# Performance work log

Measured on AMD Instinct MI355X. Metric: run time of the kernel, lower is better.

Reference implementation:

```python
import jax, jax.numpy as jnp
import numpy as np

IMAGE_SIZE = 128
FACES_PER_PIXEL = 4
BLUR_RADIUS = 0.01
EPS = 1e-8


def setup_inputs() -> dict:
    key = jax.random.key(0)
    k1, k2, k3 = jax.random.split(key, 3)
    B, V, F = 2, 2000, 800
    # verts are already projected to screen/NDC space: x,y in [-1,1], z > 0 (depth)
    xy = jax.random.uniform(k1, (B, V, 2), minval=-1.0, maxval=1.0)
    z = jax.random.uniform(k2, (B, V, 1), minval=0.5, maxval=2.5)
    verts = jnp.concatenate([xy, z], axis=-1).astype(jnp.float32)
    faces = jax.random.randint(k3, (F, 3), 0, V)
    return {"verts": verts, "faces": faces}


def _edge(a, b, p):
    # signed parallelogram area of (a -> b -> p), using xy components only
    return (p[..., 0] - a[..., 0]) * (b[..., 1] - a[..., 1]) - (
        p[..., 1] - a[..., 1]) * (b[..., 0] - a[..., 0])


def _seg_dist2(p, a, b):
    # squared distance from point p to segment [a, b] in 2D
    ab = b - a
    pa = p - a
    t = jnp.clip(jnp.sum(pa * ab, -1) / (jnp.sum(ab * ab, -1) + EPS), 0.0, 1.0)
    d = pa - t[..., None] * ab
    return jnp.sum(d * d, -1)


def _rasterize(verts, faces):
    H = W = IMAGE_SIZE
    K = FACES_PER_PIXEL
    B = verts.shape[0]
    fv = verts[:, faces]                      # [B,F,3,3] gather face vertices
    v0, v1, v2 = fv[:, :, 0], fv[:, :, 1], fv[:, :, 2]
    a0 = v0[:, None, :, :2]                   # [B,1,F,2]
    a1 = v1[:, None, :, :2]
    a2 = v2[:, None, :, :2]
    z0 = v0[:, None, :, 2]                    # [B,1,F]
    z1 = v1[:, None, :, 2]
    z2 = v2[:, None, :, 2]
    # pixel centers in NDC, pytorch3d convention: index 0 -> +1, last -> -1
    xs = 1.0 - 2.0 * (jnp.arange(W, dtype=verts.dtype) + 0.5) / W
    ys = 1.0 - 2.0 * (jnp.arange(H, dtype=verts.dtype) + 0.5) / H
    yy, xx = jnp.meshgrid(ys, xs, indexing="ij")
    p = jnp.stack([xx, yy], -1).reshape(1, -1, 1, 2)   # [1,P,1,2], P=H*W

    area = _edge(a0, a1, a2)                  # [B,1,F] signed face area*2
    w0 = _edge(a1, a2, p)                     # [B,P,F]
    w1 = _edge(a2, a0, p)
    w2 = _edge(a0, a1, p)
    denom = jnp.where(jnp.abs(area) > EPS, area,
                      jnp.where(area >= 0, EPS, -EPS))
    b0, b1, b2 = w0 / denom, w1 / denom, w2 / denom
    zpix = b0 * z0 + b1 * z1 + b2 * z2        # [B,P,F] interpolated depth

    inside = (b0 >= 0) & (b1 >= 0) & (b2 >= 0)
    dmin = jnp.minimum(_seg_dist2(p, a0, a1),
                       jnp.minimum(_seg_dist2(p, a1, a2),
                                   _seg_dist2(p, a2, a0)))
    dsign = jnp.where(inside, -dmin, dmin)    # signed squared edge distance

    valid = (inside | (dmin < BLUR_RADIUS)) & (zpix > EPS) & (
        jnp.abs(area) > EPS)
    zcand = jnp.where(valid, zpix, jnp.inf)
    _, idx = jax.lax.top_k(-zcand, K)         # K nearest faces per pixel

    take = lambda x: jnp.take_along_axis(x, idx, axis=-1)
    sel_valid = take(valid)
    pix_to_face = jnp.where(sel_valid, idx, -1)
    zbuf = jnp.where(sel_valid, take(zpix), -1.0)
    bary = jnp.stack([b0, b1, b2], -1)        # [B,P,F,3]
    bsel = jnp.take_along_axis(bary, idx[..., None], axis=2)  # [B,P,K,3]
    bsel = jnp.where(sel_valid[..., None], bsel, -1.0)
    dsel = jnp.where(sel_valid, take(dsign), -1.0)

    return (pix_to_face.reshape(B, H, W, K),
            zbuf.reshape(B, H, W, K),
            bsel.reshape(B, H, W, K, 3),
            dsel.reshape(B, H, W, K))


def reference(verts, faces):
    # Fragments: (pix_to_face, zbuf, bary_coords, dists)
    return _rasterize(verts, faces)
```

## Files before the change

kernel.cpp:

```cpp
#include <hip/hip_runtime.h>

#define IMG   128
#define KF    4
#define NF    800
#define NV    2000
#define NB    2
#define EPSF  1e-8f
#define BLURF 0.01f
#define CULL_D2 0.0103f
#define HEXT    0.0547f

typedef unsigned long long u64;
#define INVK ((((u64)0x7f800000u) << 32) | 0xffffffffu)

#pragma clang fp contract(off)

__device__ __forceinline__ float seg_d2(float pax, float pay, float abx, float aby) {
#pragma clang fp contract(off)
    float dd = (abx * abx + aby * aby) + EPSF;
    float t  = (pax * abx + pay * aby) / dd;
    t = fminf(fmaxf(t, 0.0f), 1.0f);
    float dx = pax - t * abx;
    float dy = pay - t * aby;
    return dx * dx + dy * dy;
}

__device__ __forceinline__ void ins4(u64& s0, u64& s1, u64& s2, u64& s3, u64 k) {
    bool c0 = k < s0, c1 = k < s1, c2 = k < s2, c3 = k < s3;
    s3 = c2 ? s2 : (c3 ? k : s3);
    s2 = c1 ? s1 : (c2 ? k : s2);
    s1 = c0 ? s0 : (c1 ? k : s1);
    s0 = c0 ? k  : s0;
}

__global__ __launch_bounds__(256) void raster_p1(
    const float* __restrict__ verts,
    const int*   __restrict__ faces,
    u64* __restrict__ ws,
    int sh)
{
#pragma clang fp contract(off)
    extern __shared__ char dynLDS[];
    __shared__ u64 sK[2 * 4 * 64];
    __shared__ int sTot;

    const int S     = 1 << sh;
    const int chunk = NF >> sh;
    float* sFD  = (float*)dynLDS;
    int*   sList = (int*)(dynLDS + (size_t)chunk * 10 * sizeof(float));

    const int tid   = threadIdx.x;
    const int blk   = blockIdx.x;
    const int tile  = blk >> sh;
    const int slice = blk & (S - 1);
    const int b     = tile >> 8;
    const int trow  = (tile & 255) >> 4;
    const int tcol  = tile & 15;
    const float* vb = verts + b * NV * 3;
    const int fbase = slice * chunk;

    if (tid == 0) sTot = 0;

    for (int j = tid; j < chunk; j += 256) {
        int f = fbase + j;
        int i0 = faces[3 * f + 0], i1 = faces[3 * f + 1], i2 = faces[3 * f + 2];
        float a0x = vb[3 * i0], a0y = vb[3 * i0 + 1], z0 = vb[3 * i0 + 2];
        float a1x = vb[3 * i1], a1y = vb[3 * i1 + 1], z1 = vb[3 * i1 + 2];
        float a2x = vb[3 * i2], a2y = vb[3 * i2 + 1], z2 = vb[3 * i2 + 2];
        float area = (a2x - a0x) * (a1y - a0y) - (a2y - a0y) * (a1x - a0x);
        float aab  = fabsf(area);
        float denom = (aab > EPSF) ? area : (area >= 0.0f ? EPSF : -EPSF);
        float* fd = &sFD[j * 10];
        fd[0] = a0x; fd[1] = a0y; fd[2] = a1x; fd[3] = a1y; fd[4] = a2x; fd[5] = a2y;
        fd[6] = z0;  fd[7] = z1;  fd[8] = z2;  fd[9] = denom;
    }
    __syncthreads();

    const int wave = tid >> 6;
    const int lane = tid & 63;
    const int pr = lane >> 3, pc = lane & 7;
    const int row = trow * 8 + pr, col = tcol * 8 + pc;
    const float px = 1.0f - (2.0f * ((float)col + 0.5f)) / 128.0f;
    const float py = 1.0f - (2.0f * ((float)row + 0.5f)) / 128.0f;
    const float txmax = 1.0f - (2.0f * ((float)(tcol * 8)     + 0.5f)) / 128.0f;
    const float txmin = 1.0f - (2.0f * ((float)(tcol * 8 + 7) + 0.5f)) / 128.0f;
    const float tymax = 1.0f - (2.0f * ((float)(trow * 8)     + 0.5f)) / 128.0f;
    const float tymin = 1.0f - (2.0f * ((float)(trow * 8 + 7) + 0.5f)) / 128.0f;
    const float cx = 0.5f * (txmin + txmax);
    const float cy = 0.5f * (tymin + tymax);

    for (int j = tid; j < chunk; j += 256) {
        const float* fd = &sFD[j * 10];
        float a0x = fd[0], a0y = fd[1], a1x = fd[2], a1y = fd[3], a2x = fd[4], a2y = fd[5];
        float area = (a2x - a0x) * (a1y - a0y) - (a2y - a0y) * (a1x - a0x);
        bool surv = fabsf(area) > EPSF;
        float bxmin = fminf(a0x, fminf(a1x, a2x)) - 0.101f;
        float bxmax = fmaxf(a0x, fmaxf(a1x, a2x)) + 0.101f;
        float bymin = fminf(a0y, fminf(a1y, a2y)) - 0.101f;
        float bymax = fmaxf(a0y, fmaxf(a1y, a2y)) + 0.101f;
        surv &= !(bxmin > txmax || bxmax < txmin || bymin > tymax || bymax < tymin);
        float s = (area >= 0.0f) ? 1.0f : -1.0f;
        float e0x = a2x - a1x, e0y = a2y - a1y;
        float e1x = a0x - a2x, e1y = a0y - a2y;
        float e2x = a1x - a0x, e2y = a1y - a0y;
        float w0 = s * ((cx - a1x) * e0y - (cy - a1y) * e0x) + HEXT * (fabsf(e0x) + fabsf(e0y));
        float w1 = s * ((cx - a2x) * e1y - (cy - a2y) * e1x) + HEXT * (fabsf(e1x) + fabsf(e1y));
        float w2 = s * ((cx - a0x) * e2y - (cy - a0y) * e2x) + HEXT * (fabsf(e2x) + fabsf(e2y));
        float l0 = e0x * e0x + e0y * e0y;
        float l1 = e1x * e1x + e1y * e1y;
        float l2 = e2x * e2x + e2y * e2y;
        surv &= !((w0 < 0.0f) & (w0 * w0 > CULL_D2 * l0));
        surv &= !((w1 < 0.0f) & (w1 * w1 > CULL_D2 * l1));
        surv &= !((w2 < 0.0f) & (w2 * w2 > CULL_D2 * l2));
        if (surv) {
            int pos = atomicAdd(&sTot, 1);
            sList[pos] = j;
        }
    }
    __syncthreads();
    const int total = sTot;

    u64 s0 = INVK, s1 = INVK, s2 = INVK, s3 = INVK;
    for (int j = wave; j < total; j += 4) {
        int lf = sList[j];
        const float* fd = &sFD[lf * 10];
        float a0x = fd[0], a0y = fd[1], a1x = fd[2], a1y = fd[3], a2x = fd[4], a2y = fd[5];
        float z0 = fd[6], z1 = fd[7], z2 = fd[8], denom = fd[9];
        float e0x = a2x - a1x, e0y = a2y - a1y;
        float e1x = a0x - a2x, e1y = a0y - a2y;
        float e2x = a1x - a0x, e2y = a1y - a0y;
        float p0x = px - a0x, p0y = py - a0y;
        float p1x = px - a1x, p1y = py - a1y;
        float p2x = px - a2x, p2y = py - a2y;
        float w0 = p1x * e0y - p1y * e0x;
        float w1 = p2x * e1y - p2y * e1x;
        float w2 = p0x * e2y - p0y * e2x;
        float b0 = w0 / denom, b1 = w1 / denom, b2 = w2 / denom;
        float zpix = (b0 * z0 + b1 * z1) + b2 * z2;
        bool inside = fminf(b0, fminf(b1, b2)) >= 0.0f;
        bool valid;
        if (__all(inside)) {
            valid = (zpix > EPSF);
        } else {
            float dA = seg_d2(p0x, p0y, e2x, e2y);
            float dB = seg_d2(p1x, p1y, e0x, e0y);
            float dC = seg_d2(p2x, p2y, e1x, e1y);
            float dmin = fminf(dA, fminf(dB, dC));
            valid = (inside | (dmin < BLURF)) & (zpix > EPSF);
        }
        u64 key = valid ? ((((u64)__float_as_uint(zpix)) << 32) | (unsigned)(fbase + lf)) : INVK;
        if (__any(key < s3)) ins4(s0, s1, s2, s3, key);
    }

    if (wave >= 2) {
        int r = wave - 2;
        sK[(r * 4 + 0) * 64 + lane] = s0;
        sK[(r * 4 + 1) * 64 + lane] = s1;
        sK[(r * 4 + 2) * 64 + lane] = s2;
        sK[(r * 4 + 3) * 64 + lane] = s3;
    }
    __syncthreads();
    if (wave < 2) {
        ins4(s0, s1, s2, s3, sK[(wave * 4 + 0) * 64 + lane]);
        ins4(s0, s1, s2, s3, sK[(wave * 4 + 1) * 64 + lane]);
        ins4(s0, s1, s2, s3, sK[(wave * 4 + 2) * 64 + lane]);
        ins4(s0, s1, s2, s3, sK[(wave * 4 + 3) * 64 + lane]);
    }
    __syncthreads();
    if (wave == 1) {
        sK[0 * 64 + lane] = s0;
        sK[1 * 64 + lane] = s1;
        sK[2 * 64 + lane] = s2;
        sK[3 * 64 + lane] = s3;
    }
    __syncthreads();
    if (wave == 0) {
        ins4(s0, s1, s2, s3, sK[0 * 64 + lane]);
        ins4(s0, s1, s2, s3, sK[1 * 64 + lane]);
        ins4(s0, s1, s2, s3, sK[2 * 64 + lane]);
        ins4(s0, s1, s2, s3, sK[3 * 64 + lane]);
        u64* wrow = ws + (size_t)blk * 256;
        wrow[0 * 64 + lane] = s0;
        wrow[1 * 64 + lane] = s1;
        wrow[2 * 64 + lane] = s2;
        wrow[3 * 64 + lane] = s3;
    }
}

__global__ __launch_bounds__(256) void raster_p2(
    const float* __restrict__ verts,
    const int*   __restrict__ faces,
    const u64* __restrict__ ws,
    int sh,
    float* __restrict__ out0, float* __restrict__ out1,
    float* __restrict__ out2, float* __restrict__ out3)
{
#pragma clang fp contract(off)
    __shared__ u64 sK[4 * 64];
    const int S    = 1 << sh;
    const int tid  = threadIdx.x;
    const int tile = blockIdx.x;
    const int b    = tile >> 8;
    const int trow = (tile & 255) >> 4;
    const int tcol = tile & 15;
    const float* vb = verts + b * NV * 3;

    if (tid < 64) {
        u64 s0 = INVK, s1 = INVK, s2 = INVK, s3 = INVK;
        const u64* base = ws + (size_t)tile * S * 256;
        for (int s = 0; s < S; ++s) {
            ins4(s0, s1, s2, s3, base[s * 256 + 0 * 64 + tid]);
            ins4(s0, s1, s2, s3, base[s * 256 + 1 * 64 + tid]);
            ins4(s0, s1, s2, s3, base[s * 256 + 2 * 64 + tid]);
            ins4(s0, s1, s2, s3, base[s * 256 + 3 * 64 + tid]);
        }
        sK[0 * 64 + tid] = s0;
        sK[1 * 64 + tid] = s1;
        sK[2 * 64 + tid] = s2;
        sK[3 * 64 + tid] = s3;
    }
    __syncthreads();

    int pix = tid >> 2, k = tid & 3;
    u64 key = sK[k * 64 + pix];
    int prow = pix >> 3, pcol = pix & 7;
    int grow = trow * 8 + prow, gcol = tcol * 8 + pcol;
    int p = (b * IMG + grow) * IMG + gcol;
    float qx = 1.0f - (2.0f * ((float)gcol + 0.5f)) / 128.0f;
    float qy = 1.0f - (2.0f * ((float)grow + 0.5f)) / 128.0f;
    float o0 = -1.0f, o1 = -1.0f, ob0 = -1.0f, ob1 = -1.0f, ob2 = -1.0f, o3 = -1.0f;
    if ((unsigned)(key >> 32) != 0x7f800000u) {
        int fi = (int)(unsigned)(key & 0xffffffffu);
        int i0 = faces[3 * fi + 0], i1 = faces[3 * fi + 1], i2 = faces[3 * fi + 2];
        float a0x = vb[3 * i0], a0y = vb[3 * i0 + 1], z0 = vb[3 * i0 + 2];
        float a1x = vb[3 * i1], a1y = vb[3 * i1 + 1], z1 = vb[3 * i1 + 2];
        float a2x = vb[3 * i2], a2y = vb[3 * i2 + 1], z2 = vb[3 * i2 + 2];
        float area = (a2x - a0x) * (a1y - a0y) - (a2y - a0y) * (a1x - a0x);
        float aab  = fabsf(area);
        float denom = (aab > EPSF) ? area : (area >= 0.0f ? EPSF : -EPSF);
        float e0x = a2x - a1x, e0y = a2y - a1y;
        float e1x = a0x - a2x, e1y = a0y - a2y;
        float e2x = a1x - a0x, e2y = a1y - a0y;
        float p0x = qx - a0x, p0y = qy - a0y;
        float p1x = qx - a1x, p1y = qy - a1y;
        float p2x = qx - a2x, p2y = qy - a2y;
        float w0 = p1x * e0y - p1y * e0x;
        float w1 = p2x * e1y - p2y * e1x;
        float w2 = p0x * e2y - p0y * e2x;
        float b0 = w0 / denom, b1 = w1 / denom, b2 = w2 / denom;
        float zpix = (b0 * z0 + b1 * z1) + b2 * z2;
        bool inside = (b0 >= 0.0f) & (b1 >= 0.0f) & (b2 >= 0.0f);
        float dA = seg_d2(p0x, p0y, e2x, e2y);
        float dB = seg_d2(p1x, p1y, e0x, e0y);
        float dC = seg_d2(p2x, p2y, e1x, e1y);
        float dmin = fminf(dA, fminf(dB, dC));
        o0 = (float)fi;
        o1 = zpix;
        ob0 = b0; ob1 = b1; ob2 = b2;
        o3 = inside ? -dmin : dmin;
    }
    int o = p * KF + k;
    out0[o] = o0;
    out1[o] = o1;
    out2[o * 3 + 0] = ob0;
    out2[o * 3 + 1] = ob1;
    out2[o * 3 + 2] = ob2;
    out3[o] = o3;
}

extern "C" void kernel_launch(void* const* d_in, const int* in_sizes, int n_in,
                              void* d_out, int out_size, void* d_ws, size_t ws_size,
                              hipStream_t stream) {
    const float* verts = (const float*)d_in[0];
    const int*   faces = (const int*)d_in[1];
    float* out = (float*)d_out;
    const int n0 = NB * IMG * IMG * KF;

    const size_t per_slice = 512ull * 256 * sizeof(u64);
    int sh;
    if      (ws_size >= 4 * per_slice) sh = 2;
    else if (ws_size >= 2 * per_slice) sh = 1;
    else                               sh = 0;
    const int S = 1 << sh;
    const int chunk = NF >> sh;
    const size_t dyn = (size_t)chunk * 10 * sizeof(float) + (size_t)chunk * sizeof(int);

    raster_p1<<<dim3(512 * S), dim3(256), dyn, stream>>>(verts, faces, (u64*)d_ws, sh);
    raster_p2<<<dim3(512), dim3(256), 0, stream>>>(verts, faces, (const u64*)d_ws, sh,
        out,
        out + n0,
        out + 2 * n0,
        out + 5 * n0);
}
```

Measured before the change: 95.56 us.

## Give each wave its own tile-slice with ballot/readlane face broadcast, dropping LDS

Each wavefront now independently processes one (tile, face-slice) unit instead of a block sharing an LDS face table. Faces are loaded and culled per lane, and surviving faces are broadcast to all lanes with ballot plus readlane. This removes the LDS staging, the shared atomic survivor list, the block barriers and the cross-wave top-4 merge. The face split rises to 8 slices when workspace allows, which adds parallelism but makes the second pass merge more partial lists. Each wave also redoes the vertex gathers for its own slice, and the fallback assumes the workspace holds at least 4 slices.

```diff
diff --git a/kernel.cpp b/kernel.cpp
--- a/kernel.cpp
+++ b/kernel.cpp
@@ -33,51 +33,31 @@
     s0 = c0 ? k  : s0;
 }
 
-__global__ __launch_bounds__(256) void raster_p1(
+__device__ __forceinline__ float bcastf(float v, int s) {
+    return __uint_as_float((unsigned)__builtin_amdgcn_readlane(__float_as_uint(v), s));
+}
+
+__global__ __launch_bounds__(256, 4) void raster_p1(
     const float* __restrict__ verts,
     const int*   __restrict__ faces,
     u64* __restrict__ ws,
     int sh)
 {
 #pragma clang fp contract(off)
-    extern __shared__ char dynLDS[];
-    __shared__ u64 sK[2 * 4 * 64];
-    __shared__ int sTot;
-
     const int S     = 1 << sh;
     const int chunk = NF >> sh;
-    float* sFD  = (float*)dynLDS;
-    int*   sList = (int*)(dynLDS + (size_t)chunk * 10 * sizeof(float));
-
     const int tid   = threadIdx.x;
-    const int blk   = blockIdx.x;
-    const int tile  = blk >> sh;
-    const int slice = blk & (S - 1);
+    const int wave  = tid >> 6;
+    const int lane  = tid & 63;
+    const int unit  = blockIdx.x * 4 + wave;
+    const int tile  = unit >> sh;
+    const int slice = unit & (S - 1);
     const int b     = tile >> 8;
     const int trow  = (tile & 255) >> 4;
     const int tcol  = tile & 15;
     const float* vb = verts + b * NV * 3;
     const int fbase = slice * chunk;
 
-    if (tid == 0) sTot = 0;
-
-    for (int j = tid; j < chunk; j += 256) {
-        int f = fbase + j;
-        int i0 = faces[3 * f + 0], i1 = faces[3 * f + 1], i2 = faces[3 * f + 2];
-        float a0x = vb[3 * i0], a0y = vb[3 * i0 + 1], z0 = vb[3 * i0 + 2];
-        float a1x = vb[3 * i1], a1y = vb[3 * i1 + 1], z1 = vb[3 * i1 + 2];
-        float a2x = vb[3 * i2], a2y = vb[3 * i2 + 1], z2 = vb[3 * i2 + 2];
-        float area = (a2x - a0x) * (a1y - a0y) - (a2y - a0y) * (a1x - a0x);
-        float aab  = fabsf(area);
-        float denom = (aab > EPSF) ? area : (area >= 0.0f ? EPSF : -EPSF);
-        float* fd = &sFD[j * 10];
-        fd[0] = a0x; fd[1] = a0y; fd[2] = a1x; fd[3] = a1y; fd[4] = a2x; fd[5] = a2y;
-        fd[6] = z0;  fd[7] = z1;  fd[8] = z2;  fd[9] = denom;
-    }
-    __syncthreads();
-
-    const int wave = tid >> 6;
-    const int lane = tid & 63;
     const int pr = lane >> 3, pc = lane & 7;
     const int row = trow * 8 + pr, col = tcol * 8 + pc;
     const float px = 1.0f - (2.0f * ((float)col + 0.5f)) / 128.0f;
@@ -89,102 +69,84 @@
     const float cx = 0.5f * (txmin + txmax);
     const float cy = 0.5f * (tymin + tymax);
 
-    for (int j = tid; j < chunk; j += 256) {
-        const float* fd = &sFD[j * 10];
-        float a0x = fd[0], a0y = fd[1], a1x = fd[2], a1y = fd[3], a2x = fd[4], a2y = fd[5];
-        float area = (a2x - a0x) * (a1y - a0y) - (a2y - a0y) * (a1x - a0x);
-        bool surv = fabsf(area) > EPSF;
-        float bxmin = fminf(a0x, fminf(a1x, a2x)) - 0.101f;
-        float bxmax = fmaxf(a0x, fmaxf(a1x, a2x)) + 0.101f;
-        float bymin = fminf(a0y, fminf(a1y, a2y)) - 0.101f;
-        float bymax = fmaxf(a0y, fmaxf(a1y, a2y)) + 0.101f;
-        surv &= !(bxmin > txmax || bxmax < txmin || bymin > tymax || bymax < tymin);
-        float s = (area >= 0.0f) ? 1.0f : -1.0f;
-        float e0x = a2x - a1x, e0y = a2y - a1y;
-        float e1x = a0x - a2x, e1y = a0y - a2y;
-        float e2x = a1x - a0x, e2y = a1y - a0y;
-        float w0 = s * ((cx - a1x) * e0y - (cy - a1y) * e0x) + HEXT * (fabsf(e0x) + fabsf(e0y));
-        float w1 = s * ((cx - a2x) * e1y - (cy - a2y) * e1x) + HEXT * (fabsf(e1x) + fabsf(e1y));
-        float w2 = s * ((cx - a0x) * e2y - (cy - a0y) * e2x) + HEXT * (fabsf(e2x) + fabsf(e2y));
-        float l0 = e0x * e0x + e0y * e0y;
-        float l1 = e1x * e1x + e1y * e1y;
-        float l2 = e2x * e2x + e2y * e2y;
-        surv &= !((w0 < 0.0f) & (w0 * w0 > CULL_D2 * l0));
-        surv &= !((w1 < 0.0f) & (w1 * w1 > CULL_D2 * l1));
-        surv &= !((w2 < 0.0f) & (w2 * w2 > CULL_D2 * l2));
-        if (surv) {
-            int pos = atomicAdd(&sTot, 1);
-            sList[pos] = j;
+    u64 s0 = INVK, s1 = INVK, s2 = INVK, s3 = INVK;
+
+    for (int fo = 0; fo < chunk; fo += 64) {
+        const int fl = fo + lane;
+        bool surv = false;
+        float a0x = 0, a0y = 0, a1x = 0, a1y = 0, a2x = 0, a2y = 0;
+        float z0 = 0, z1 = 0, z2 = 0, denom = 1;
+        if (fl < chunk) {
+            const int f = fbase + fl;
+            int i0 = faces[3 * f + 0], i1 = faces[3 * f + 1], i2 = faces[3 * f + 2];
+            a0x = vb[3 * i0]; a0y = vb[3 * i0 + 1]; z0 = vb[3 * i0 + 2];
+            a1x = vb[3 * i1]; a1y = vb[3 * i1 + 1]; z1 = vb[3 * i1 + 2];
+            a2x = vb[3 * i2]; a2y = vb[3 * i2 + 1]; z2 = vb[3 * i2 + 2];
+            float area = (a2x - a0x) * (a1y - a0y) - (a2y - a0y) * (a1x - a0x);
+            float aab  = fabsf(area);
+            denom = (aab > EPSF) ? area : (area >= 0.0f ? EPSF : -EPSF);
+            surv = aab > EPSF;
+            float bxmin = fminf(a0x, fminf(a1x, a2x)) - 0.101f;
+            float bxmax = fmaxf(a0x, fmaxf(a1x, a2x)) + 0.101f;
+            float bymin = fminf(a0y, fminf(a1y, a2y)) - 0.101f;
+            float bymax = fmaxf(a0y, fmaxf(a1y, a2y)) + 0.101f;
+            surv &= !(bxmin > txmax || bxmax < txmin || bymin > tymax || bymax < tymin);
+            float s = (area >= 0.0f) ? 1.0f : -1.0f;
+            float e0x = a2x - a1x, e0y = a2y - a1y;
+            float e1x = a0x - a2x, e1y = a0y - a2y;
+            float e2x = a1x - a0x, e2y = a1y - a0y;
+            float w0 = s * ((cx - a1x) * e0y - (cy - a1y) * e0x) + HEXT * (fabsf(e0x) + fabsf(e0y));
+            float w1 = s * ((cx - a2x) * e1y - (cy - a2y) * e1x) + HEXT * (fabsf(e1x) + fabsf(e1y));
+            float w2 = s * ((cx - a0x) * e2y - (cy - a0y) * e2x) + HEXT * (fabsf(e2x) + fabsf(e2y));
+            float l0 = e0x * e0x + e0y * e0y;
+            float l1 = e1x * e1x + e1y * e1y;
+            float l2 = e2x * e2x + e2y * e2y;
+            surv &= !((w0 < 0.0f) & (w0 * w0 > CULL_D2 * l0));
+            surv &= !((w1 < 0.0f) & (w1 * w1 > CULL_D2 * l1));
+            surv &= !((w2 < 0.0f) & (w2 * w2 > CULL_D2 * l2));
+        }
+        u64 mask = __ballot(surv);
+        while (mask) {
+            const int sl = (int)__builtin_ctzll(mask);
+            mask &= mask - 1;
+            float A0x = bcastf(a0x, sl), A0y = bcastf(a0y, sl);
+            float A1x = bcastf(a1x, sl), A1y = bcastf(a1y, sl);
+            float A2x = bcastf(a2x, sl), A2y = bcastf(a2y, sl);
+            float Z0  = bcastf(z0, sl),  Z1  = bcastf(z1, sl);
+            float Z2  = bcastf(z2, sl),  D   = bcastf(denom, sl);
+            const int fg = fbase + fo + sl;
+            float e0x = A2x - A1x, e0y = A2y - A1y;
+            float e1x = A0x - A2x, e1y = A0y - A2y;
+            float e2x = A1x - A0x, e2y = A1y - A0y;
+            float p0x = px - A0x, p0y = py - A0y;
+            float p1x = px - A1x, p1y = py - A1y;
+            float p2x = px - A2x, p2y = py - A2y;
+            float w0 = p1x * e0y - p1y * e0x;
+            float w1 = p2x * e1y - p2y * e1x;
+            float w2 = p0x * e2y - p0y * e2x;
+            float b0 = w0 / D, b1 = w1 / D, b2 = w2 / D;
+            float zpix = (b0 * Z0 + b1 * Z1) + b2 * Z2;
+            bool inside = fminf(b0, fminf(b1, b2)) >= 0.0f;
+            bool valid;
+            if (__all(inside)) {
+                valid = (zpix > EPSF);
+            } else {
+                float dA = seg_d2(p0x, p0y, e2x, e2y);
+                float dB = seg_d2(p1x, p1y, e0x, e0y);
+                float dC = seg_d2(p2x, p2y, e1x, e1y);
+                float dmin = fminf(dA, fminf(dB, dC));
+                valid = (inside | (dmin < BLURF)) & (zpix > EPSF);
+            }
+            u64 key = valid ? ((((u64)__float_as_uint(zpix)) << 32) | (unsigned)fg) : INVK;
+            if (__any(key < s3)) ins4(s0, s1, s2, s3, key);
         }
     }
-    __syncthreads();
-    const int total = sTot;
-
-    u64 s0 = INVK, s1 = INVK, s2 = INVK, s3 = INVK;
-    for (int j = wave; j < total; j += 4) {
-        int lf = sList[j];
-        const float* fd = &sFD[lf * 10];
-        float a0x = fd[0], a0y = fd[1], a1x = fd[2], a1y = fd[3], a2x = fd[4], a2y = fd[5];
-        float z0 = fd[6], z1 = fd[7], z2 = fd[8], denom = fd[9];
-        float e0x = a2x - a1x, e0y = a2y - a1y;
-        float e1x = a0x - a2x, e1y = a0y - a2y;
-        float e2x = a1x - a0x, e2y = a1y - a0y;
-        float p0x = px - a0x, p0y = py - a0y;
-        float p1x = px - a1x, p1y = py - a1y;
-        float p2x = px - a2x, p2y = py - a2y;
-        float w0 = p1x * e0y - p1y * e0x;
-        float w1 = p2x * e1y - p2y * e1x;
-        float w2 = p0x * e2y - p0y * e2x;
-        float b0 = w0 / denom, b1 = w1 / denom, b2 = w2 / denom;
-        float zpix = (b0 * z0 + b1 * z1) + b2 * z2;
-        bool inside = fminf(b0, fminf(b1, b2)) >= 0.0f;
-        bool valid;
-        if (__all(inside)) {
-            valid = (zpix > EPSF);
-        } else {
-            float dA = seg_d2(p0x, p0y, e2x, e2y);
-            float dB = seg_d2(p1x, p1y, e0x, e0y);
-            float dC = seg_d2(p2x, p2y, e1x, e1y);
-            float dmin = fminf(dA, fminf(dB, dC));
-            valid = (inside | (dmin < BLURF)) & (zpix > EPSF);
-        }
-        u64 key = valid ? ((((u64)__float_as_uint(zpix)) << 32) | (unsigned)(fbase + lf)) : INVK;
-        if (__any(key < s3)) ins4(s0, s1, s2, s3, key);
-    }
-
-    if (wave >= 2) {
-        int r = wave - 2;
-        sK[(r * 4 + 0) * 64 + lane] = s0;
-        sK[(r * 4 + 1) * 64 + lane] = s1;
-        sK[(r * 4 + 2) * 64 + lane] = s2;
-        sK[(r * 4 + 3) * 64 + lane] = s3;
-    }
-    __syncthreads();
-    if (wave < 2) {
-        ins4(s0, s1, s2, s3, sK[(wave * 4 + 0) * 64 + lane]);
-        ins4(s0, s1, s2, s3, sK[(wave * 4 + 1) * 64 + lane]);
-        ins4(s0, s1, s2, s3, sK[(wave * 4 + 2) * 64 + lane]);
-        ins4(s0, s1, s2, s3, sK[(wave * 4 + 3) * 64 + lane]);
-    }
-    __syncthreads();
-    if (wave == 1) {
-        sK[0 * 64 + lane] = s0;
-        sK[1 * 64 + lane] = s1;
-        sK[2 * 64 + lane] = s2;
-        sK[3 * 64 + lane] = s3;
-    }
-    __syncthreads();
-    if (wave == 0) {
-        ins4(s0, s1, s2, s3, sK[0 * 64 + lane]);
-        ins4(s0, s1, s2, s3, sK[1 * 64 + lane]);
-        ins4(s0, s1, s2, s3, sK[2 * 64 + lane]);
-        ins4(s0, s1, s2, s3, sK[3 * 64 + lane]);
-        u64* wrow = ws + (size_t)blk * 256;
-        wrow[0 * 64 + lane] = s0;
-        wrow[1 * 64 + lane] = s1;
-        wrow[2 * 64 + lane] = s2;
-        wrow[3 * 64 + lane] = s3;
-    }
+
+    u64* wrow = ws + (size_t)unit * 256;
+    wrow[0 * 64 + lane] = s0;
+    wrow[1 * 64 + lane] = s1;
+    wrow[2 * 64 + lane] = s2;
+    wrow[3 * 64 + lane] = s3;
 }
 
 __global__ __launch_bounds__(256) void raster_p2(
@@ -276,16 +238,12 @@
     float* out = (float*)d_out;
     const int n0 = NB * IMG * IMG * KF;
 
-    const size_t per_slice = 512ull * 256 * sizeof(u64);
-    int sh;
-    if      (ws_size >= 4 * per_slice) sh = 2;
-    else if (ws_size >= 2 * per_slice) sh = 1;
-    else                               sh = 0;
+    const size_t per_unit = 256 * sizeof(u64);
+    int sh = (ws_size >= 512ull * 8 * per_unit) ? 3
+           : 2;
     const int S = 1 << sh;
-    const int chunk = NF >> sh;
-    const size_t dyn = (size_t)chunk * 10 * sizeof(float) + (size_t)chunk * sizeof(int);
-
-    raster_p1<<<dim3(512 * S), dim3(256), dyn, stream>>>(verts, faces, (u64*)d_ws, sh);
+
+    raster_p1<<<dim3(512 * S / 4), dim3(256), 0, stream>>>(verts, faces, (u64*)d_ws, sh);
     raster_p2<<<dim3(512), dim3(256), 0, stream>>>(verts, faces, (const u64*)d_ws, sh,
         out,
         out + n0,
```

Result: slower. 106.7 us (+11.7%).
